# Performance work log

Hardware: AMD Instinct MI355X
Metric: run time of the kernel (lower is better)

Reference implementation:

```python
import jax, jax.numpy as jnp
import numpy as np

B = 16384  # batch size
NP = 49    # 7x7 patches


def _attn(Q, K, V):
    # Faithful to the torch loop: token[i] = Q[i].T @ K[i] / sqrt(S) @ V[i].T, then permute.
    # Note dk = Q.size(1) == 49 (seq len), NOT the head dim — preserved here.
    scale = 1.0 / jnp.asarray(Q.shape[1], Q.dtype) ** 0.5  # 1/7
    S = jnp.einsum('bsd,bse->bde', Q, K) * scale           # (B, d, d)
    # (S @ V^T)^T  ->  out[b,s,d] = sum_e S[b,d,e] * V[b,s,e]
    return jnp.einsum('bde,bse->bsd', S, V)                # (B, 49, d)


def setup_inputs() -> dict:
    key = jax.random.key(0)
    ks = jax.random.split(key, 12)
    s = 0.1  # init scale for weights
    return {
        'x':       jax.random.normal(ks[0], (B, 3, 28, 28), dtype=jnp.float32),
        'pos_emb': jax.random.uniform(ks[1], (7, 7, 16), dtype=jnp.float32),  # torch.rand
        'WQ1': jax.random.normal(ks[2], (NP, 16, 32), dtype=jnp.float32) * s,
        'WK1': jax.random.normal(ks[3], (NP, 16, 32), dtype=jnp.float32) * s,
        'WV1': jax.random.normal(ks[4], (NP, 16, 32), dtype=jnp.float32) * s,
        'WQ2': jax.random.normal(ks[5], (NP, 8, 16), dtype=jnp.float32) * s,
        'WK2': jax.random.normal(ks[6], (NP, 8, 16), dtype=jnp.float32) * s,
        'WV2': jax.random.normal(ks[7], (NP, 8, 16), dtype=jnp.float32) * s,
        'fc1_w': jax.random.normal(ks[8], (16, NP * 8), dtype=jnp.float32) * s,
        'fc1_b': jnp.zeros((16,), dtype=jnp.float32),
        'fc2_w': jax.random.normal(ks[9], (10, 16), dtype=jnp.float32) * s,
        'fc2_b': jnp.zeros((10,), dtype=jnp.float32),
    }


def reference(x, pos_emb, WQ1, WK1, WV1, WQ2, WK2, WV2, fc1_w, fc1_b, fc2_w, fc2_b):
    b = x.shape[0]
    # grayscale (x has 3 channels)
    g = 0.299 * x[:, 0] + 0.587 * x[:, 1] + 0.114 * x[:, 2]   # (B, 28, 28)
    # 7x7 grid of 4x4 patches, flattened row-major within each patch
    patches = g.reshape(b, 7, 4, 7, 4).transpose(0, 1, 3, 2, 4).reshape(b, NP, 16)
    pe = jnp.broadcast_to(pos_emb.reshape(1, NP, 16), (b, NP, 16))
    tok1 = jnp.concatenate([patches, pe], axis=-1)            # (B, 49, 32)

    # 49 independent per-patch projections, batched: y[:,s,:] = tok[:,s,:] @ W[s].T
    Q1 = jnp.einsum('bsi,soi->bso', tok1, WQ1)
    K1 = jnp.einsum('bsi,soi->bso', tok1, WK1)
    V1 = jnp.einsum('bsi,soi->bso', tok1, WV1)
    tok2 = jax.nn.softmax(_attn(Q1, K1, V1), axis=-1)         # (B, 49, 16)

    Q2 = jnp.einsum('bsi,soi->bso', tok2, WQ2)
    K2 = jnp.einsum('bsi,soi->bso', tok2, WK2)
    V2 = jnp.einsum('bsi,soi->bso', tok2, WV2)
    tok3 = jax.nn.softmax(_attn(Q2, K2, V2), axis=-1)         # (B, 49, 8)

    flat = tok3.reshape(b, NP * 8)
    h = jax.nn.relu(flat @ fc1_w.T + fc1_b)
    return jax.nn.softmax(h @ fc2_w.T + fc2_b, axis=-1)       # (B, 10)
```

## Files before the change

### kernel.cpp

```cpp
#include <hip/hip_runtime.h>
#include <cstdint>

typedef unsigned int u32;
typedef unsigned short u16;
typedef _Float16 h2 __attribute__((ext_vector_type(2)));
typedef float f32x4 __attribute__((ext_vector_type(4)));

#define WS_W1A   0
#define WS_W1B   37632
#define WS_CQ    75264
#define WS_W2A   84672
#define WS_W2B   103488
#define WS_F1H   122304
#define WS_F1B   134848
#define WS_F2W   134912
#define WS_F2B   135552

__device__ __forceinline__ u32 packh2(float a, float b) {
  h2 h; h.x = (_Float16)a; h.y = (_Float16)b;
  return __builtin_bit_cast(u32, h);
}
__device__ __forceinline__ float dot2u(u32 a, u32 b, float c) {
#if __has_builtin(__builtin_amdgcn_fdot2)
  return __builtin_amdgcn_fdot2(__builtin_bit_cast(h2, a), __builtin_bit_cast(h2, b), c, false);
#else
  h2 ha = __builtin_bit_cast(h2, a), hb = __builtin_bit_cast(h2, b);
  return c + (float)ha.x * (float)hb.x + (float)ha.y * (float)hb.y;
#endif
}
__device__ __forceinline__ float dot16(const u32* t, uint4 a, uint4 b, float c) {
  c = dot2u(t[0], a.x, c); c = dot2u(t[1], a.y, c);
  c = dot2u(t[2], a.z, c); c = dot2u(t[3], a.w, c);
  c = dot2u(t[4], b.x, c); c = dot2u(t[5], b.y, c);
  c = dot2u(t[6], b.z, c); c = dot2u(t[7], b.w, c);
  return c;
}

__device__ __forceinline__ f32x4 ldnt(const float* p) {
  return __builtin_nontemporal_load((const f32x4*)p);
}

__device__ __forceinline__ void wfence() {
  __builtin_amdgcn_sched_barrier(0);
  asm volatile("s_waitcnt lgkmcnt(0)" ::: "memory");
  __builtin_amdgcn_sched_barrier(0);
}

extern "C" __global__ void vit_prep(
    const float* __restrict__ pe,
    const float* __restrict__ wq1, const float* __restrict__ wk1, const float* __restrict__ wv1,
    const float* __restrict__ wq2, const float* __restrict__ wk2, const float* __restrict__ wv2,
    const float* __restrict__ fw1, const float* __restrict__ fb1,
    const float* __restrict__ fw2, const float* __restrict__ fb2,
    char* __restrict__ ws)
{
  const int t = blockIdx.x * 256 + threadIdx.x;
  _Float16* w1aH = (_Float16*)(ws + WS_W1A);
  _Float16* w1bH = (_Float16*)(ws + WS_W1B);
  float*    cq   = (float*)(ws + WS_CQ);
  _Float16* w2aH = (_Float16*)(ws + WS_W2A);
  _Float16* w2bH = (_Float16*)(ws + WS_W2B);
  u32* f1h = (u32*)(ws + WS_F1H);
  float* o1b = (float*)(ws + WS_F1B);
  float* o2w = (float*)(ws + WS_F2W);
  float* o2b = (float*)(ws + WS_F2B);

  if (t < 2352) {
    int p = t / 784, rem = t % 784;
    int o = rem / 49, s = rem % 49;
    const float* W = (p == 0 ? wq1 : (p == 1 ? wk1 : wv1)) + s*512 + o*32;
    float sc = (p == 0) ? (1.0f/7.0f) : 1.0f;
    #pragma unroll
    for (int i = 0; i < 8; ++i) w1aH[t*8 + i] = (_Float16)(W[i] * sc);
    #pragma unroll
    for (int i = 0; i < 8; ++i) w1bH[t*8 + i] = (_Float16)(W[8 + i] * sc);
    float acc = 0.f;
    #pragma unroll
    for (int i = 0; i < 16; ++i) acc += pe[s*16 + i] * W[16 + i];
    cq[t] = acc * sc;
  } else if (t < 3528) {
    int u = t - 2352;
    int p = u / 392, rem = u % 392;
    int o = rem / 49, s = rem % 49;
    const float* W = (p == 0 ? wq2 : (p == 1 ? wk2 : wv2)) + s*128 + o*16;
    float sc = (p == 0) ? (1.0f/7.0f) : 1.0f;
    #pragma unroll
    for (int i = 0; i < 8; ++i) w2aH[u*8 + i] = (_Float16)(W[i] * sc);
    #pragma unroll
    for (int i = 0; i < 8; ++i) w2bH[u*8 + i] = (_Float16)(W[8 + i] * sc);
  } else if (t < 6664) {
    int u = t - 3528;
    int h = u / 196, jc = u % 196;
    f1h[u] = packh2(fw1[h*392 + 2*jc], fw1[h*392 + 2*jc + 1]);
  } else if (t < 6680) {
    int u = t - 6664; o1b[u] = fb1[u];
  } else if (t < 6840) {
    int u = t - 6680; o2w[u] = fw2[u];
  } else if (t < 6850) {
    int u = t - 6840; o2b[u] = fb2[u];
  }
}

extern "C" __global__ void __launch_bounds__(256, 2)
vit_main(const float* __restrict__ x, const char* __restrict__ ws, float* __restrict__ out)
{
  __shared__ uint4 smem4[32768 / 16];
  char* smem = (char*)smem4;
  const u32 tid  = threadIdx.x;
  const u32 lane = tid & 63u;
  const u32 wv   = tid >> 6;

  const uint4* g1a = (const uint4*)(ws + WS_W1A);
  const uint4* g1b = (const uint4*)(ws + WS_W1B);
  const float* gcq = (const float*)(ws + WS_CQ);
  const uint4* g2a = (const uint4*)(ws + WS_W2A);
  const uint4* g2b = (const uint4*)(ws + WS_W2B);
  const uint4* f1hg = (const uint4*)(ws + WS_F1H);
  const float* f1bg = (const float*)(ws + WS_F1B);
  const float* f2wg = (const float*)(ws + WS_F2W);
  const float* f2bg = (const float*)(ws + WS_F2B);

  char* pw = smem + wv * 8192;
  const u32 s = lane;
  const u32 pr = s / 7u, pc = s - pr * 7u;

  const u32 bbase = blockIdx.x * 8u + wv * 2u;

  u32 p2h[2][8];
  u32 v1h[2][8];
  u32 th4[2][8];
  u32 v2h[2][4];

  if (s < 49u) {
    #pragma unroll
    for (int u = 0; u < 2; ++u) {
      const float* xb = x + (size_t)(bbase + u) * 2352u;
      #pragma unroll
      for (int r = 0; r < 4; ++r) {
        const float* rp = xb + (4u*pr + r) * 28u + 4u*pc;
        f32x4 rr = ldnt(rp);
        f32x4 gg = ldnt(rp + 784);
        f32x4 bb = ldnt(rp + 1568);
        float g0 = 0.299f*rr.x + 0.587f*gg.x + 0.114f*bb.x;
        float g1 = 0.299f*rr.y + 0.587f*gg.y + 0.114f*bb.y;
        float g2 = 0.299f*rr.z + 0.587f*gg.z + 0.114f*bb.z;
        float g3 = 0.299f*rr.w + 0.587f*gg.w + 0.114f*bb.w;
        p2h[u][r*2]   = packh2(g0, g1);
        p2h[u][r*2+1] = packh2(g2, g3);
      }
    }
  }

  struct WSet { uint4 a0, b0, a1, b1; float c0, c1; };
  if (s < 49u) {
    const int si = (int)s;
    WSet A, B, C;
#define P2LOAD(S, J) do { \
    const int rr_ = ((J)/3)*98 + si + (((J)%3)==0 ? 0 : (((J)%3)==1 ? 784 : 1568)); \
    S.a0 = g1a[rr_]; S.b0 = g1b[rr_]; S.a1 = g1a[rr_+49]; S.b1 = g1b[rr_+49]; \
    S.c0 = gcq[rr_]; S.c1 = gcq[rr_+49]; } while (0)
#define P2COMP(S, J) do { \
    const int o_ = 2*((J)/3); \
    if (((J)%3) == 0) { \
      _Float16* q0_ = (_Float16*)pw; \
      _Float16* q1_ = (_Float16*)(pw + 4096); \
      q0_[o_*56 + s]     = (_Float16)dot16(p2h[0], S.a0, S.b0, S.c0); \
      q0_[(o_+1)*56 + s] = (_Float16)dot16(p2h[0], S.a1, S.b1, S.c1); \
      q1_[o_*56 + s]     = (_Float16)dot16(p2h[1], S.a0, S.b0, S.c0); \
      q1_[(o_+1)*56 + s] = (_Float16)dot16(p2h[1], S.a1, S.b1, S.c1); \
    } else if (((J)%3) == 1) { \
      _Float16* k0_ = (_Float16*)(pw + 1792); \
      _Float16* k1_ = (_Float16*)(pw + 4096 + 1792); \
      k0_[o_*56 + s]     = (_Float16)dot16(p2h[0], S.a0, S.b0, S.c0); \
      k0_[(o_+1)*56 + s] = (_Float16)dot16(p2h[0], S.a1, S.b1, S.c1); \
      k1_[o_*56 + s]     = (_Float16)dot16(p2h[1], S.a0, S.b0, S.c0); \
      k1_[(o_+1)*56 + s] = (_Float16)dot16(p2h[1], S.a1, S.b1, S.c1); \
    } else { \
      v1h[0][(J)/3] = packh2(dot16(p2h[0], S.a0, S.b0, S.c0), dot16(p2h[0], S.a1, S.b1, S.c1)); \
      v1h[1][(J)/3] = packh2(dot16(p2h[1], S.a0, S.b0, S.c0), dot16(p2h[1], S.a1, S.b1, S.c1)); \
    } } while (0)
#define P2STEP(LS, CS, J) do { P2LOAD(LS, (J)+2); \
    __builtin_amdgcn_sched_barrier(0); P2COMP(CS, J); } while (0)
    P2LOAD(A, 0); P2LOAD(B, 1);
    P2STEP(C,A,0);  P2STEP(A,B,1);  P2STEP(B,C,2);
    P2STEP(C,A,3);  P2STEP(A,B,4);  P2STEP(B,C,5);
    P2STEP(C,A,6);  P2STEP(A,B,7);  P2STEP(B,C,8);
    P2STEP(C,A,9);  P2STEP(A,B,10); P2STEP(B,C,11);
    P2STEP(C,A,12); P2STEP(A,B,13); P2STEP(B,C,14);
    P2STEP(C,A,15); P2STEP(A,B,16); P2STEP(B,C,17);
    P2STEP(C,A,18); P2STEP(A,B,19); P2STEP(B,C,20);
    P2STEP(C,A,21);
    __builtin_amdgcn_sched_barrier(0); P2COMP(B, 22);
    __builtin_amdgcn_sched_barrier(0); P2COMP(C, 23);
#undef P2STEP
#undef P2COMP
#undef P2LOAD
  }
  wfence();

  {
    const u32 d2 = lane >> 3, e2 = lane & 7u;
    #pragma unroll
    for (int u = 0; u < 2; ++u) {
      char* su = pw + u*4096;
      const u32* qw = (const u32*)su;
      const u32* kw = (const u32*)(su + 1792);
      const u32* qA = qw + (2u*d2) * 28u;
      const u32* qB = qA + 28u;
      const u32* kA = kw + (2u*e2) * 28u;
      const u32* kB = kA + 28u;
      float a00 = 0.f, a01 = 0.f, a10 = 0.f, a11 = 0.f;
      #pragma unroll
      for (int t7 = 0; t7 < 6; ++t7) {
        uint4 qa = *(const uint4*)(qA + 4*t7);
        uint4 qb = *(const uint4*)(qB + 4*t7);
        uint4 ka = *(const uint4*)(kA + 4*t7);
        uint4 kb = *(const uint4*)(kB + 4*t7);
        a00 = dot2u(qa.x, ka.x, a00); a00 = dot2u(qa.y, ka.y, a00);
        a00 = dot2u(qa.z, ka.z, a00); a00 = dot2u(qa.w, ka.w, a00);
        a01 = dot2u(qa.x, kb.x, a01); a01 = dot2u(qa.y, kb.y, a01);
        a01 = dot2u(qa.z, kb.z, a01); a01 = dot2u(qa.w, kb.w, a01);
        a10 = dot2u(qb.x, ka.x, a10); a10 = dot2u(qb.y, ka.y, a10);
        a10 = dot2u(qb.z, ka.z, a10); a10 = dot2u(qb.w, ka.w, a10);
        a11 = dot2u(qb.x, kb.x, a11); a11 = dot2u(qb.y, kb.y, a11);
        a11 = dot2u(qb.z, kb.z, a11); a11 = dot2u(qb.w, kb.w, a11);
      }
      {
        float q0t = (float)((const _Float16*)qA)[48];
        float q1t = (float)((const _Float16*)qB)[48];
        float k0t = (float)((const _Float16*)kA)[48];
        float k1t = (float)((const _Float16*)kB)[48];
        a00 = fmaf(q0t, k0t, a00); a01 = fmaf(q0t, k1t, a01);
        a10 = fmaf(q1t, k0t, a10); a11 = fmaf(q1t, k1t, a11);
      }
      u32* s1 = (u32*)(su + 3584);
      s1[(2u*d2)*8u + e2]   = packh2(a00, a01);
      s1[(2u*d2+1)*8u + e2] = packh2(a10, a11);
    }
  }
  wfence();

  if (s < 49u) {
    #pragma unroll
    for (int u = 0; u < 2; ++u) {
      char* su = pw + u*4096;
      const u32* s1 = (const u32*)(su + 3584);
      float od[16];
      #pragma unroll
      for (int d = 0; d < 16; ++d) {
        uint4 sa = *(const uint4*)&s1[d*8];
        uint4 sb = *(const uint4*)&s1[d*8 + 4];
        float acc = dot2u(sa.x, v1h[u][0], 0.f);
        acc = dot2u(sa.y, v1h[u][1], acc);
        acc = dot2u(sa.z, v1h[u][2], acc);
        acc = dot2u(sa.w, v1h[u][3], acc);
        acc = dot2u(sb.x, v1h[u][4], acc);
        acc = dot2u(sb.y, v1h[u][5], acc);
        acc = dot2u(sb.z, v1h[u][6], acc);
        acc = dot2u(sb.w, v1h[u][7], acc);
        od[d] = acc;
      }
      float m = od[0];
      #pragma unroll
      for (int d = 1; d < 16; ++d) m = fmaxf(m, od[d]);
      float sum = 0.f;
      #pragma unroll
      for (int d = 0; d < 16; ++d) { od[d] = __expf(od[d] - m); sum += od[d]; }
      float rs = 1.0f / sum;
      #pragma unroll
      for (int j = 0; j < 8; ++j) th4[u][j] = packh2(od[2*j]*rs, od[2*j+1]*rs);
    }
  }

  if (s < 49u) {
    const int si = (int)s;
    struct WSet2 { uint4 a0, b0, a1, b1; };
    WSet2 A, B, C;
#define P4LOAD(S, J) do { \
    const int rr_ = ((J)/3)*98 + si + (((J)%3)==0 ? 0 : (((J)%3)==1 ? 392 : 784)); \
    S.a0 = g2a[rr_]; S.b0 = g2b[rr_]; S.a1 = g2a[rr_+49]; S.b1 = g2b[rr_+49]; } while (0)
#define P4COMP(S, J) do { \
    const int o_ = 2*((J)/3); \
    if (((J)%3) == 0) { \
      _Float16* q0_ = (_Float16*)pw; \
      _Float16* q1_ = (_Float16*)(pw + 4096); \
      q0_[o_*56 + s]     = (_Float16)dot16(th4[0], S.a0, S.b0, 0.f); \
      q0_[(o_+1)*56 + s] = (_Float16)dot16(th4[0], S.a1, S.b1, 0.f); \
      q1_[o_*56 + s]     = (_Float16)dot16(th4[1], S.a0, S.b0, 0.f); \
      q1_[(o_+1)*56 + s] = (_Float16)dot16(th4[1], S.a1, S.b1, 0.f); \
    } else if (((J)%3) == 1) { \
      _Float16* k0_ = (_Float16*)(pw + 896); \
      _Float16* k1_ = (_Float16*)(pw + 4096 + 896); \
      k0_[o_*56 + s]     = (_Float16)dot16(th4[0], S.a0, S.b0, 0.f); \
      k0_[(o_+1)*56 + s] = (_Float16)dot16(th4[0], S.a1, S.b1, 0.f); \
      k1_[o_*56 + s]     = (_Float16)dot16(th4[1], S.a0, S.b0, 0.f); \
      k1_[(o_+1)*56 + s] = (_Float16)dot16(th4[1], S.a1, S.b1, 0.f); \
    } else { \
      v2h[0][(J)/3] = packh2(dot16(th4[0], S.a0, S.b0, 0.f), dot16(th4[0], S.a1, S.b1, 0.f)); \
      v2h[1][(J)/3] = packh2(dot16(th4[1], S.a0, S.b0, 0.f), dot16(th4[1], S.a1, S.b1, 0.f)); \
    } } while (0)
#define P4STEP(LS, CS, J) do { P4LOAD(LS, (J)+2); \
    __builtin_amdgcn_sched_barrier(0); P4COMP(CS, J); } while (0)
    P4LOAD(A, 0); P4LOAD(B, 1);
    P4STEP(C,A,0); P4STEP(A,B,1); P4STEP(B,C,2);
    P4STEP(C,A,3); P4STEP(A,B,4); P4STEP(B,C,5);
    P4STEP(C,A,6); P4STEP(A,B,7); P4STEP(B,C,8);
    P4STEP(C,A,9);
    __builtin_amdgcn_sched_barrier(0); P4COMP(B, 10);
    __builtin_amdgcn_sched_barrier(0); P4COMP(C, 11);
#undef P4STEP
#undef P4COMP
#undef P4LOAD
  }
  wfence();

  {
    const u32 uu = lane >> 5, d = (lane >> 2) & 7u, e2 = lane & 3u;
    char* su = pw + uu*4096;
    const u32* qw = (const u32*)su;
    const u32* kw = (const u32*)(su + 896);
    const u32* qA = qw + d * 28u;
    const u32* kA = kw + (2u*e2) * 28u;
    const u32* kB = kA + 28u;
    float a0 = 0.f, a1 = 0.f;
    #pragma unroll
    for (int t7 = 0; t7 < 6; ++t7) {
      uint4 qa = *(const uint4*)(qA + 4*t7);
      uint4 ka = *(const uint4*)(kA + 4*t7);
      uint4 kb = *(const uint4*)(kB + 4*t7);
      a0 = dot2u(qa.x, ka.x, a0); a0 = dot2u(qa.y, ka.y, a0);
      a0 = dot2u(qa.z, ka.z, a0); a0 = dot2u(qa.w, ka.w, a0);
      a1 = dot2u(qa.x, kb.x, a1); a1 = dot2u(qa.y, kb.y, a1);
      a1 = dot2u(qa.z, kb.z, a1); a1 = dot2u(qa.w, kb.w, a1);
    }
    {
      float qt = (float)((const _Float16*)qA)[48];
      float k0t = (float)((const _Float16*)kA)[48];
      float k1t = (float)((const _Float16*)kB)[48];
      a0 = fmaf(qt, k0t, a0); a1 = fmaf(qt, k1t, a1);
    }
    u32* s2 = (u32*)(su + 3584);
    s2[d*4u + e2] = packh2(a0, a1);
  }
  wfence();

  if (s < 49u) {
    #pragma unroll
    for (int u = 0; u < 2; ++u) {
      char* su = pw + u*4096;
      const u32* s2 = (const u32*)(su + 3584);
      float od[8];
      #pragma unroll
      for (int d = 0; d < 8; ++d) {
        uint4 sr = *(const uint4*)&s2[d*4];
        float acc = dot2u(sr.x, v2h[u][0], 0.f);
        acc = dot2u(sr.y, v2h[u][1], acc);
        acc = dot2u(sr.z, v2h[u][2], acc);
        acc = dot2u(sr.w, v2h[u][3], acc);
        od[d] = acc;
      }
      float m = od[0];
      #pragma unroll
      for (int d = 1; d < 8; ++d) m = fmaxf(m, od[d]);
      float sum = 0.f;
      #pragma unroll
      for (int d = 0; d < 8; ++d) { od[d] = __expf(od[d] - m); sum += od[d]; }
      float rs = 1.0f / sum;
      uint4 tw;
      tw.x = packh2(od[0]*rs, od[1]*rs);
      tw.y = packh2(od[2]*rs, od[3]*rs);
      tw.z = packh2(od[4]*rs, od[5]*rs);
      tw.w = packh2(od[6]*rs, od[7]*rs);
      *(uint4*)((u32*)su + s*4u) = tw;
    }
  }
  wfence();

  {
    const u32 uu = lane >> 5, h = (lane >> 1) & 15u, half = lane & 1u;
    char* su = pw + uu*4096;
    const u32* t3 = (const u32*)su;
    float acc = half ? 0.f : f1bg[h];
    #pragma unroll
    for (int jj = 0; jj < 25; ++jj) {
      int j = (int)(half * 25u) + jj;
      if (j < 49) {
        uint4 tj = *(const uint4*)&t3[j*4];
        uint4 wj = f1hg[h*49u + (u32)j];
        acc = dot2u(tj.x, wj.x, acc);
        acc = dot2u(tj.y, wj.y, acc);
        acc = dot2u(tj.z, wj.z, acc);
        acc = dot2u(tj.w, wj.w, acc);
      }
    }
    float* prt = (float*)(su + 3584 + 192);
    prt[h*2u + half] = acc;
  }
  wfence();

  {
    const u32 uu = lane >> 5, c = lane & 31u;
    char* su = pw + uu*4096;
    if (c < 10u) {
      const float4* pv4 = (const float4*)(su + 3584 + 192);
      float hb[16];
      #pragma unroll
      for (int g = 0; g < 8; ++g) {
        float4 pv = pv4[g];
        hb[2*g]   = fmaxf(pv.x + pv.y, 0.f);
        hb[2*g+1] = fmaxf(pv.z + pv.w, 0.f);
      }
      const float* wr = f2wg + c*16u;
      float acc = f2bg[c];
      #pragma unroll
      for (int h = 0; h < 16; ++h) acc = fmaf(hb[h], wr[h], acc);
      float* lg = (float*)(su + 3584 + 384);
      lg[c] = acc;
    }
  }
  wfence();

  {
    const u32 uu = lane >> 5, c = lane & 31u;
    char* su = pw + uu*4096;
    if (c < 10u) {
      const float* lg = (const float*)(su + 3584 + 384);
      float mx = lg[0];
      #pragma unroll
      for (int i = 1; i < 10; ++i) mx = fmaxf(mx, lg[i]);
      float sum = 0.f;
      #pragma unroll
      for (int i = 0; i < 10; ++i) sum += __expf(lg[i] - mx);
      out[(size_t)(bbase + uu) * 10u + c] = __expf(lg[c] - mx) / sum;
    }
  }
}

extern "C" void kernel_launch(void* const* d_in, const int* in_sizes, int n_in,
                              void* d_out, int out_size, void* d_ws, size_t ws_size,
                              hipStream_t stream)
{
  const float* x   = (const float*)d_in[0];
  const float* pe  = (const float*)d_in[1];
  const float* wq1 = (const float*)d_in[2];
  const float* wk1 = (const float*)d_in[3];
  const float* wv1 = (const float*)d_in[4];
  const float* wq2 = (const float*)d_in[5];
  const float* wk2 = (const float*)d_in[6];
  const float* wv2 = (const float*)d_in[7];
  const float* f1w = (const float*)d_in[8];
  const float* f1b = (const float*)d_in[9];
  const float* f2w = (const float*)d_in[10];
  const float* f2b = (const float*)d_in[11];
  char* ws = (char*)d_ws;
  float* out = (float*)d_out;

  hipLaunchKernelGGL(vit_prep, dim3(27), dim3(256), 0, stream,
                     pe, wq1, wk1, wv1, wq2, wk2, wv2, f1w, f1b, f2w, f2b, ws);
  hipLaunchKernelGGL(vit_main, dim3(2048), dim3(256), 0, stream, x, ws, out);
}
```

Measured before the change: 282.0 us.

## Compute layer-1 QKV projections with MFMA across block-shared grayscale patches

```diff
diff --git a/kernel.cpp b/kernel.cpp
--- a/kernel.cpp
+++ b/kernel.cpp
@@ -4,6 +4,7 @@
 typedef unsigned int u32;
 typedef unsigned short u16;
 typedef _Float16 h2 __attribute__((ext_vector_type(2)));
+typedef _Float16 v8h __attribute__((ext_vector_type(8)));
 typedef float f32x4 __attribute__((ext_vector_type(4)));
 
 #define WS_W1A   0
@@ -104,14 +105,12 @@
 extern "C" __global__ void __launch_bounds__(256, 2)
 vit_main(const float* __restrict__ x, const char* __restrict__ ws, float* __restrict__ out)
 {
-  __shared__ uint4 smem4[32768 / 16];
+  __shared__ uint4 smem4[45312 / 16];
   char* smem = (char*)smem4;
   const u32 tid  = threadIdx.x;
   const u32 lane = tid & 63u;
   const u32 wv   = tid >> 6;
 
-  const uint4* g1a = (const uint4*)(ws + WS_W1A);
-  const uint4* g1b = (const uint4*)(ws + WS_W1B);
   const float* gcq = (const float*)(ws + WS_CQ);
   const uint4* g2a = (const uint4*)(ws + WS_W2A);
   const uint4* g2b = (const uint4*)(ws + WS_W2B);
@@ -120,24 +119,26 @@
   const float* f2wg = (const float*)(ws + WS_F2W);
   const float* f2bg = (const float*)(ws + WS_F2B);
 
-  char* pw = smem + wv * 8192;
+  char* gbase = smem;
+  char* pw = smem + 12544 + wv * 8192;
   const u32 s = lane;
-  const u32 pr = s / 7u, pc = s - pr * 7u;
 
   const u32 bbase = blockIdx.x * 8u + wv * 2u;
 
-  u32 p2h[2][8];
-  u32 v1h[2][8];
   u32 th4[2][8];
   u32 v2h[2][4];
 
-  if (s < 49u) {
-    #pragma unroll
-    for (int u = 0; u < 2; ++u) {
-      const float* xb = x + (size_t)(bbase + u) * 2352u;
+  #pragma unroll
+  for (int it = 0; it < 2; ++it) {
+    const int p = (int)tid + it*256;
+    if (p < 392) {
+      const int b = p / 49, ps = p - b*49;
+      const int pr = ps / 7, pc = ps - pr*7;
+      const float* xb = x + (size_t)(blockIdx.x * 8u + (u32)b) * 2352u;
+      u32 og[8];
       #pragma unroll
       for (int r = 0; r < 4; ++r) {
-        const float* rp = xb + (4u*pr + r) * 28u + 4u*pc;
+        const float* rp = xb + (4*pr + r) * 28 + 4*pc;
         f32x4 rr = ldnt(rp);
         f32x4 gg = ldnt(rp + 784);
         f32x4 bb = ldnt(rp + 1568);
@@ -145,58 +146,52 @@
         float g1 = 0.299f*rr.y + 0.587f*gg.y + 0.114f*bb.y;
         float g2 = 0.299f*rr.z + 0.587f*gg.z + 0.114f*bb.z;
         float g3 = 0.299f*rr.w + 0.587f*gg.w + 0.114f*bb.w;
-        p2h[u][r*2]   = packh2(g0, g1);
-        p2h[u][r*2+1] = packh2(g2, g3);
-      }
-    }
-  }
-
-  struct WSet { uint4 a0, b0, a1, b1; float c0, c1; };
-  if (s < 49u) {
-    const int si = (int)s;
-    WSet A, B, C;
-#define P2LOAD(S, J) do { \
-    const int rr_ = ((J)/3)*98 + si + (((J)%3)==0 ? 0 : (((J)%3)==1 ? 784 : 1568)); \
-    S.a0 = g1a[rr_]; S.b0 = g1b[rr_]; S.a1 = g1a[rr_+49]; S.b1 = g1b[rr_+49]; \
-    S.c0 = gcq[rr_]; S.c1 = gcq[rr_+49]; } while (0)
-#define P2COMP(S, J) do { \
-    const int o_ = 2*((J)/3); \
-    if (((J)%3) == 0) { \
-      _Float16* q0_ = (_Float16*)pw; \
-      _Float16* q1_ = (_Float16*)(pw + 4096); \
-      q0_[o_*56 + s]     = (_Float16)dot16(p2h[0], S.a0, S.b0, S.c0); \
-      q0_[(o_+1)*56 + s] = (_Float16)dot16(p2h[0], S.a1, S.b1, S.c1); \
-      q1_[o_*56 + s]     = (_Float16)dot16(p2h[1], S.a0, S.b0, S.c0); \
-      q1_[(o_+1)*56 + s] = (_Float16)dot16(p2h[1], S.a1, S.b1, S.c1); \
-    } else if (((J)%3) == 1) { \
-      _Float16* k0_ = (_Float16*)(pw + 1792); \
-      _Float16* k1_ = (_Float16*)(pw + 4096 + 1792); \
-      k0_[o_*56 + s]     = (_Float16)dot16(p2h[0], S.a0, S.b0, S.c0); \
-      k0_[(o_+1)*56 + s] = (_Float16)dot16(p2h[0], S.a1, S.b1, S.c1); \
-      k1_[o_*56 + s]     = (_Float16)dot16(p2h[1], S.a0, S.b0, S.c0); \
-      k1_[(o_+1)*56 + s] = (_Float16)dot16(p2h[1], S.a1, S.b1, S.c1); \
-    } else { \
-      v1h[0][(J)/3] = packh2(dot16(p2h[0], S.a0, S.b0, S.c0), dot16(p2h[0], S.a1, S.b1, S.c1)); \
-      v1h[1][(J)/3] = packh2(dot16(p2h[1], S.a0, S.b0, S.c0), dot16(p2h[1], S.a1, S.b1, S.c1)); \
-    } } while (0)
-#define P2STEP(LS, CS, J) do { P2LOAD(LS, (J)+2); \
-    __builtin_amdgcn_sched_barrier(0); P2COMP(CS, J); } while (0)
-    P2LOAD(A, 0); P2LOAD(B, 1);
-    P2STEP(C,A,0);  P2STEP(A,B,1);  P2STEP(B,C,2);
-    P2STEP(C,A,3);  P2STEP(A,B,4);  P2STEP(B,C,5);
-    P2STEP(C,A,6);  P2STEP(A,B,7);  P2STEP(B,C,8);
-    P2STEP(C,A,9);  P2STEP(A,B,10); P2STEP(B,C,11);
-    P2STEP(C,A,12); P2STEP(A,B,13); P2STEP(B,C,14);
-    P2STEP(C,A,15); P2STEP(A,B,16); P2STEP(B,C,17);
-    P2STEP(C,A,18); P2STEP(A,B,19); P2STEP(B,C,20);
-    P2STEP(C,A,21);
-    __builtin_amdgcn_sched_barrier(0); P2COMP(B, 22);
-    __builtin_amdgcn_sched_barrier(0); P2COMP(C, 23);
-#undef P2STEP
-#undef P2COMP
-#undef P2LOAD
-  }
-  wfence();
+        og[r*2]   = packh2(g0, g1);
+        og[r*2+1] = packh2(g2, g3);
+      }
+      uint4* gq = (uint4*)(gbase + b*1568 + ps*32);
+      gq[0] = make_uint4(og[0], og[1], og[2], og[3]);
+      gq[1] = make_uint4(og[4], og[5], og[6], og[7]);
+    }
+  }
+  __syncthreads();
+
+  {
+    const int o  = (int)(lane & 15u);
+    const int ck = (int)(lane >> 4);
+    const int s0 = (int)wv * 13;
+    const int s1 = (s0 + 13 < 49) ? s0 + 13 : 49;
+    const char* wrow = ws + WS_W1A + (size_t)ck * 37632;
+    #pragma unroll 1
+    for (int sp = s0; sp < s1; ++sp) {
+      const int r0 = o*49 + sp;
+      v8h av = (v8h)0, bq = (v8h)0, bk = (v8h)0, bv = (v8h)0;
+      if (ck < 2) {
+        av = *(const v8h*)(gbase + ((size_t)(o & 7))*1568 + sp*32 + ck*16);
+        bq = *(const v8h*)(wrow + (size_t)r0*16);
+        bk = *(const v8h*)(wrow + (size_t)(r0 + 784)*16);
+        bv = *(const v8h*)(wrow + (size_t)(r0 + 1568)*16);
+      }
+      const float cq0 = gcq[r0], ck0 = gcq[r0 + 784], cv0 = gcq[r0 + 1568];
+      f32x4 cQ = {cq0, cq0, cq0, cq0};
+      f32x4 cK = {ck0, ck0, ck0, ck0};
+      f32x4 cV = {cv0, cv0, cv0, cv0};
+      f32x4 dq = __builtin_amdgcn_mfma_f32_16x16x32_f16(av, bq, cQ, 0, 0, 0);
+      f32x4 dk = __builtin_amdgcn_mfma_f32_16x16x32_f16(av, bk, cK, 0, 0, 0);
+      f32x4 dv = __builtin_amdgcn_mfma_f32_16x16x32_f16(av, bv, cV, 0, 0, 0);
+      if (ck < 2) {
+        #pragma unroll
+        for (int j = 0; j < 4; ++j) {
+          const int b = ck*4 + j;
+          char* reg = smem + 12544 + (size_t)b * 4096;
+          ((_Float16*)reg)[o*56 + sp]          = (_Float16)dq[j];
+          ((_Float16*)(reg + 1792))[o*56 + sp] = (_Float16)dk[j];
+          ((_Float16*)(gbase + (size_t)b*1568 + sp*32))[o] = (_Float16)dv[j];
+        }
+      }
+    }
+  }
+  __syncthreads();
 
   {
     const u32 d2 = lane >> 3, e2 = lane & 7u;
@@ -245,19 +240,21 @@
     for (int u = 0; u < 2; ++u) {
       char* su = pw + u*4096;
       const u32* s1 = (const u32*)(su + 3584);
+      const uint4* vv = (const uint4*)(gbase + (size_t)(wv*2u + u)*1568 + s*32u);
+      uint4 v0 = vv[0], v1 = vv[1];
       float od[16];
       #pragma unroll
       for (int d = 0; d < 16; ++d) {
         uint4 sa = *(const uint4*)&s1[d*8];
         uint4 sb = *(const uint4*)&s1[d*8 + 4];
-        float acc = dot2u(sa.x, v1h[u][0], 0.f);
-        acc = dot2u(sa.y, v1h[u][1], acc);
-        acc = dot2u(sa.z, v1h[u][2], acc);
-        acc = dot2u(sa.w, v1h[u][3], acc);
-        acc = dot2u(sb.x, v1h[u][4], acc);
-        acc = dot2u(sb.y, v1h[u][5], acc);
-        acc = dot2u(sb.z, v1h[u][6], acc);
-        acc = dot2u(sb.w, v1h[u][7], acc);
+        float acc = dot2u(sa.x, v0.x, 0.f);
+        acc = dot2u(sa.y, v0.y, acc);
+        acc = dot2u(sa.z, v0.z, acc);
+        acc = dot2u(sa.w, v0.w, acc);
+        acc = dot2u(sb.x, v1.x, acc);
+        acc = dot2u(sb.y, v1.y, acc);
+        acc = dot2u(sb.z, v1.z, acc);
+        acc = dot2u(sb.w, v1.w, acc);
         od[d] = acc;
       }
       float m = od[0];
```

Result: slower. 303.6 us (+7.7%).
